# Kernel optimization log

Measured on AMD Instinct MI355X. Metric: run time of the kernel, lower is better.

The kernel has to match this reference:

```python
import jax, jax.numpy as jnp
import numpy as np

N = 50000        # nodes
E = 800000       # edges (avg degree 16)
H = 128          # hidden_nf
IN_NODE = 11     # in_node_nf
IN_EDGE = 4      # in_edge_nf
L = 4            # n_layers


def _lin_init(key, fan_in, fan_out, layers=None):
    shape = (fan_in, fan_out) if layers is None else (layers, fan_in, fan_out)
    return jax.random.normal(key, shape, dtype=jnp.float32) / np.sqrt(fan_in)


def setup_inputs() -> dict:
    key = jax.random.key(0)
    ks = jax.random.split(key, 16)
    edge_in = 2 * H + 1 + IN_EDGE   # [h_row, h_col, radial, edge_attr]
    node_in = H + H + IN_NODE       # [h, agg, h0]
    return {
        "h0": jax.random.normal(ks[0], (N, IN_NODE), dtype=jnp.float32),
        "x": jax.random.normal(ks[1], (N, 3), dtype=jnp.float32),
        "edge_index": jax.random.randint(ks[2], (2, E), 0, N),
        "edge_attr": jax.random.normal(ks[3], (E, IN_EDGE), dtype=jnp.float32),
        "node_mask": jnp.ones((N, 1), dtype=jnp.float32),
        "edge_mask": jnp.ones((E, 1), dtype=jnp.float32),
        "n_nodes": N,
        "emb_w": _lin_init(ks[4], IN_NODE, H),
        "emb_b": jnp.zeros((H,), dtype=jnp.float32),
        "ew1": _lin_init(ks[5], edge_in, H, L),
        "eb1": jnp.zeros((L, H), dtype=jnp.float32),
        "ew2": _lin_init(ks[6], H, H, L),
        "eb2": jnp.zeros((L, H), dtype=jnp.float32),
        "nw1": _lin_init(ks[7], node_in, H, L),
        "nb1": jnp.zeros((L, H), dtype=jnp.float32),
        "nw2": _lin_init(ks[8], H, H, L),
        "nb2": jnp.zeros((L, H), dtype=jnp.float32),
    }


def reference(h0, x, edge_index, edge_attr, node_mask, edge_mask, n_nodes,
              emb_w, emb_b, ew1, eb1, ew2, eb2, nw1, nb1, nw2, nb2):
    row, col = edge_index[0], edge_index[1]
    num_nodes = h0.shape[0]
    # coord2radial (coords never updated since coord_model is not called)
    coord_diff = x[row] - x[col]                               # [E, 3]
    radial = jnp.sum(coord_diff * coord_diff, axis=1, keepdims=True)  # [E, 1]

    h = h0 @ emb_w + emb_b                                     # embedding, [N, H]
    for i in range(L):
        # edge model
        edge_in = jnp.concatenate([h[row], h[col], radial, edge_attr], axis=1)
        m = jax.nn.silu(edge_in @ ew1[i] + eb1[i])
        m = jax.nn.silu(m @ ew2[i] + eb2[i])
        m = m * edge_mask                                      # [E, H]
        # node model: scatter-sum messages, concat with h and node_attr=h0
        agg = jax.ops.segment_sum(m, row, num_segments=num_nodes)  # [N, H]
        node_in = jnp.concatenate([h, agg, h0], axis=1)
        out = jax.nn.silu(node_in @ nw1[i] + nb1[i]) @ nw2[i] + nb2[i]
        h = h + out                                            # recurrent residual
    return h
```

## Files before the change

kernel.cpp:

```cpp
#include <hip/hip_runtime.h>

#define NN 50000
#define NE 800000
#define HD 128
#define INN 11
#define NL 4
#define NG16 3125
#define BTS 132
#define K1S 292
#define NB  196

typedef __attribute__((ext_vector_type(8))) short bf16x8;
typedef __attribute__((ext_vector_type(4))) float f32x4;
typedef __attribute__((ext_vector_type(2))) float f32x2;

__device__ __forceinline__ float silu_f(float x) {
    return x * __builtin_amdgcn_rcpf(1.0f + __expf(-x));
}

__device__ __forceinline__ short f2bf(float x) {
    unsigned u = __float_as_uint(x);
    return (short)((u + 0x7FFFu + ((u >> 16) & 1u)) >> 16);
}
__device__ __forceinline__ unsigned f2bf2u(float lo, float hi) {
    unsigned a = __float_as_uint(lo), b = __float_as_uint(hi);
    a = (a + 0x7FFFu + ((a >> 16) & 1u)) >> 16;
    b = (b + 0x7FFFu + ((b >> 16) & 1u)) & 0xFFFF0000u;
    return a | b;
}
__device__ __forceinline__ bf16x8 pack8(float4 a, float4 b) {
    bf16x8 r;
    r[0] = f2bf(a.x); r[1] = f2bf(a.y); r[2] = f2bf(a.z); r[3] = f2bf(a.w);
    r[4] = f2bf(b.x); r[5] = f2bf(b.y); r[6] = f2bf(b.z); r[7] = f2bf(b.w);
    return r;
}

__global__ __launch_bounds__(256) void embed_kernel(
    const float* __restrict__ h0, const float* __restrict__ w,
    const float* __restrict__ b, float* __restrict__ h)
{
    int idx = blockIdx.x * 256 + threadIdx.x;
    if (idx >= NN * HD) return;
    int n = idx >> 7, j = idx & 127;
    float acc = b[j];
    #pragma unroll
    for (int k = 0; k < INN; ++k)
        acc += h0[n * INN + k] * w[k * HD + j];
    h[idx] = acc;
}

__global__ __launch_bounds__(256) void csr_zero(int* __restrict__ cnt)
{
    int i = blockIdx.x * 256 + threadIdx.x;
    if (i < NN) cnt[i] = 0;
}

__global__ __launch_bounds__(256) void csr_hist(const int* __restrict__ ei, int* __restrict__ cnt)
{
    int e = blockIdx.x * 256 + threadIdx.x;
    atomicAdd(&cnt[ei[e]], 1);
}

__global__ __launch_bounds__(256) void csr_blocksum(
    const int* __restrict__ cnt, int* __restrict__ bsum)
{
    __shared__ int red[4];
    int j = blockIdx.x * 256 + threadIdx.x;
    int v = (j < NN) ? cnt[j] : 0;
    #pragma unroll
    for (int off = 1; off < 64; off <<= 1) v += __shfl_xor(v, off, 64);
    int lane = threadIdx.x & 63, wv = threadIdx.x >> 6;
    if (lane == 0) red[wv] = v;
    __syncthreads();
    if (threadIdx.x == 0)
        bsum[blockIdx.x] = red[0] + red[1] + red[2] + red[3];
}

__global__ __launch_bounds__(256) void csr_scanpart(
    const int* __restrict__ bsum, int* __restrict__ boff, int* __restrict__ rowptr)
{
    __shared__ int part[256];
    int t = threadIdx.x;
    int v = (t < NB) ? bsum[t] : 0;
    part[t] = v;
    __syncthreads();
    #pragma unroll
    for (int off = 1; off < 256; off <<= 1) {
        int tmp = (t >= off) ? part[t - off] : 0;
        __syncthreads();
        part[t] += tmp;
        __syncthreads();
    }
    if (t < NB) boff[t] = part[t] - v;
    if (t == NB - 1) rowptr[NN] = part[t];
}

__global__ __launch_bounds__(256) void csr_emit(
    const int* __restrict__ cnt, const int* __restrict__ boff,
    int* __restrict__ rowptr, int* __restrict__ cursor)
{
    __shared__ int part[256];
    int t = threadIdx.x;
    int j = blockIdx.x * 256 + t;
    int v = (j < NN) ? cnt[j] : 0;
    part[t] = v;
    __syncthreads();
    #pragma unroll
    for (int off = 1; off < 256; off <<= 1) {
        int tmp = (t >= off) ? part[t - off] : 0;
        __syncthreads();
        part[t] += tmp;
        __syncthreads();
    }
    if (j < NN) {
        int r = boff[blockIdx.x] + part[t] - v;
        rowptr[j] = r;
        cursor[j] = r;
    }
}

__global__ __launch_bounds__(256) void csr_fill(
    const int* __restrict__ ei, int* __restrict__ cursor, int* __restrict__ eidx)
{
    int e = blockIdx.x * 256 + threadIdx.x;
    int r = ei[e];
    int p = atomicAdd(&cursor[r], 1);
    eidx[p] = e;
}

__global__ __launch_bounds__(256) void edge_pre(
    const int* __restrict__ ei, const int* __restrict__ eidx,
    const float* __restrict__ x, const float* __restrict__ emask,
    int4* __restrict__ ed_p)
{
    int p = blockIdx.x * 256 + threadIdx.x;
    int e = eidx[p];
    int r = ei[e], c = ei[NE + e];
    float dx = x[3 * r]     - x[3 * c];
    float dy = x[3 * r + 1] - x[3 * c + 1];
    float dz = x[3 * r + 2] - x[3 * c + 2];
    float rad = dx * dx + dy * dy + dz * dz;
    ed_p[p] = make_int4(r * 64, c * 64, __float_as_int(rad), __float_as_int(emask[e]));
}

__global__ __launch_bounds__(1024) void vpad_zero(unsigned* __restrict__ vb32)
{
    vb32[(size_t)NE * 64 + threadIdx.x] = 0u;
}

__global__ __launch_bounds__(512) void tu_mfma(
    const float* __restrict__ h, const float* __restrict__ ew1_l,
    const float* __restrict__ eb1_l,
    short* __restrict__ tb, short* __restrict__ ub)
{
    __shared__ __align__(16) short BT[128 * BTS];
    const float* wsrc = ew1_l + (blockIdx.y ? 128 * HD : 0);
    short* outp = blockIdx.y ? ub : tb;
    for (int i = threadIdx.x; i < 128 * 128; i += 512) {
        int c = i >> 7, k = i & 127;
        BT[c * BTS + k] = f2bf(wsrc[k * HD + c]);
    }
    int wv = threadIdx.x >> 6, lane = threadIdx.x & 63;
    int ln15 = lane & 15, quad = lane >> 4;
    __syncthreads();

    for (int g = blockIdx.x * 8 + wv; g < NG16; g += gridDim.x * 8) {
        int row = g * 16 + ln15;
        const float* hrow = h + row * HD;
        bf16x8 afr[4];
        #pragma unroll
        for (int kt = 0; kt < 4; ++kt) {
            float4 x0 = *(const float4*)(hrow + kt * 32 + quad * 8);
            float4 x1 = *(const float4*)(hrow + kt * 32 + quad * 8 + 4);
            afr[kt] = pack8(x0, x1);
        }
        #pragma unroll
        for (int ct = 0; ct < 8; ++ct) {
            f32x4 acc = {0.f, 0.f, 0.f, 0.f};
            #pragma unroll
            for (int kt = 0; kt < 4; ++kt) {
                bf16x8 bfr = *(const bf16x8*)&BT[(ct * 16 + ln15) * BTS + kt * 32 + quad * 8];
                acc = __builtin_amdgcn_mfma_f32_16x16x32_bf16(afr[kt], bfr, acc, 0, 0, 0);
            }
            int col = ct * 16 + ln15;
            float bb = blockIdx.y ? 0.f : eb1_l[col];
            #pragma unroll
            for (int r4 = 0; r4 < 4; ++r4) {
                int orow = g * 16 + quad * 4 + r4;
                outp[orow * HD + col] = f2bf(acc[r4] + bb);
            }
        }
    }
}

__global__ __launch_bounds__(512) void edge_v_kernel(
    const short* __restrict__ tb, const short* __restrict__ ub,
    const int4* __restrict__ ed_p, const int* __restrict__ eidx,
    const float* __restrict__ eattr,
    const float* __restrict__ ew1_l,
    short* __restrict__ vbuf)
{
    int cp = threadIdx.x & 63;
    int c0 = cp * 2;
    f32x2 wr2  = *(const f32x2*)&ew1_l[256 * HD + c0];
    f32x2 wa02 = *(const f32x2*)&ew1_l[257 * HD + c0];
    f32x2 wa12 = *(const f32x2*)&ew1_l[258 * HD + c0];
    f32x2 wa22 = *(const f32x2*)&ew1_l[259 * HD + c0];
    f32x2 wa32 = *(const f32x2*)&ew1_l[260 * HD + c0];

    const unsigned* tb32 = (const unsigned*)tb;
    const unsigned* ub32 = (const unsigned*)ub;
    const float4*   ea4  = (const float4*)eattr;
    unsigned*       vb32 = (unsigned*)vbuf;

    int w  = (blockIdx.x * 512 + threadIdx.x) >> 6;
    int nw = gridDim.x * 8;

    for (int p0 = w * 4; p0 < NE; p0 += nw * 4) {
        int4 edv[4]; unsigned twv[4], uwv[4]; float4 eav[4];
        #pragma unroll
        for (int j = 0; j < 4; ++j) edv[j] = ed_p[p0 + j];
        #pragma unroll
        for (int j = 0; j < 4; ++j) {
            twv[j] = tb32[edv[j].x + cp];
            uwv[j] = ub32[edv[j].y + cp];
            eav[j] = ea4[eidx[p0 + j]];
        }
        #pragma unroll
        for (int j = 0; j < 4; ++j) {
            float rad = __int_as_float(edv[j].z);
            f32x2 s;
            s.x = __uint_as_float(twv[j] << 16)        + __uint_as_float(uwv[j] << 16);
            s.y = __uint_as_float(twv[j] & 0xFFFF0000u) + __uint_as_float(uwv[j] & 0xFFFF0000u);
            s += rad * wr2;
            s += eav[j].x * wa02;
            s += eav[j].y * wa12;
            s += eav[j].z * wa22;
            s += eav[j].w * wa32;
            vb32[(size_t)(p0 + j) * 64 + cp] = f2bf2u(silu_f(s.x), silu_f(s.y));
        }
    }
}

__global__ __launch_bounds__(512) void edge_agg_kernel(
    const short* __restrict__ vbuf, const int4* __restrict__ ed_p,
    const int* __restrict__ rowptr,
    const float* __restrict__ ew2_l, const float* __restrict__ eb2_l,
    short* __restrict__ aggb)
{
    __shared__ __align__(16) short BT[128 * BTS];
    __shared__ float s_b2[128];

    for (int i = threadIdx.x; i < 128 * 128; i += 512) {
        int k = i >> 7, n = i & 127;
        BT[n * BTS + k] = f2bf(ew2_l[i]);
    }
    if (threadIdx.x < 128) s_b2[threadIdx.x] = eb2_l[threadIdx.x];

    int lane = threadIdx.x & 63;
    int wv   = threadIdx.x >> 6;
    int ln15 = lane & 15;
    int quad = lane >> 4;
    __syncthreads();

    for (int n = blockIdx.x * 8 + wv; n < NN; n += gridDim.x * 8) {
        int s = rowptr[n], en = rowptr[n + 1];

        float sums[8];
        #pragma unroll
        for (int ct = 0; ct < 8; ++ct) sums[ct] = 0.f;

        for (int base = s; base < en; base += 16) {
            const short* vrow = vbuf + (size_t)(base + ln15) * HD + quad * 8;
            bf16x8 afr[4];
            #pragma unroll
            for (int kt = 0; kt < 4; ++kt)
                afr[kt] = *(const bf16x8*)(vrow + kt * 32);

            int pr = base + quad * 4;
            float mk0 = (pr + 0 < en) ? __int_as_float(ed_p[pr + 0].w) : 0.f;
            float mk1 = (pr + 1 < en) ? __int_as_float(ed_p[pr + 1].w) : 0.f;
            float mk2 = (pr + 2 < en) ? __int_as_float(ed_p[pr + 2].w) : 0.f;
            float mk3 = (pr + 3 < en) ? __int_as_float(ed_p[pr + 3].w) : 0.f;

            #pragma unroll
            for (int ct = 0; ct < 8; ++ct) {
                f32x4 acc = {0.f, 0.f, 0.f, 0.f};
                #pragma unroll
                for (int kt = 0; kt < 4; ++kt) {
                    bf16x8 bfr = *(const bf16x8*)&BT[(ct * 16 + ln15) * BTS + kt * 32 + quad * 8];
                    acc = __builtin_amdgcn_mfma_f32_16x16x32_bf16(afr[kt], bfr, acc, 0, 0, 0);
                }
                float b2c = s_b2[ct * 16 + ln15];
                sums[ct] += silu_f(acc[0] + b2c) * mk0 + silu_f(acc[1] + b2c) * mk1
                          + silu_f(acc[2] + b2c) * mk2 + silu_f(acc[3] + b2c) * mk3;
            }
        }

        #pragma unroll
        for (int ct = 0; ct < 8; ++ct) {
            float v = sums[ct];
            v += __shfl_xor(v, 16, 64);
            v += __shfl_xor(v, 32, 64);
            sums[ct] = v;
        }
        float vA = (quad & 2) ? ((quad & 1) ? sums[6] : sums[4])
                              : ((quad & 1) ? sums[2] : sums[0]);
        float vB = (quad & 2) ? ((quad & 1) ? sums[7] : sums[5])
                              : ((quad & 1) ? sums[3] : sums[1]);
        int colA = quad * 32 + ln15;
        aggb[(size_t)n * HD + colA]      = f2bf(vA);
        aggb[(size_t)n * HD + colA + 16] = f2bf(vB);
    }
}

__global__ __launch_bounds__(512) void nk1_mfma(
    const float* __restrict__ h, const short* __restrict__ aggb,
    const float* __restrict__ h0,
    const float* __restrict__ nw1_l, const float* __restrict__ nb1_l,
    short* __restrict__ qb)
{
    __shared__ __align__(16) short BT[64 * K1S];
    int c0 = blockIdx.y * 64;
    for (int i = threadIdx.x; i < 64 * 288; i += 512) {
        int c = i / 288, k = i - c * 288;
        BT[c * K1S + k] = (k < 267) ? f2bf(nw1_l[k * HD + c0 + c]) : (short)0;
    }
    int wv = threadIdx.x >> 6, lane = threadIdx.x & 63;
    int ln15 = lane & 15, quad = lane >> 4;
    __syncthreads();

    for (int g = blockIdx.x * 8 + wv; g < NG16; g += gridDim.x * 8) {
        int row = g * 16 + ln15;
        const float* hrow = h + row * HD;
        bf16x8 afr[9];
        #pragma unroll
        for (int kt = 0; kt < 4; ++kt) {
            float4 x0 = *(const float4*)(hrow + kt * 32 + quad * 8);
            float4 x1 = *(const float4*)(hrow + kt * 32 + quad * 8 + 4);
            afr[kt] = pack8(x0, x1);
        }
        #pragma unroll
        for (int kt = 0; kt < 4; ++kt)
            afr[4 + kt] = *(const bf16x8*)(aggb + (size_t)row * HD + kt * 32 + quad * 8);
        {
            bf16x8 a8 = {0, 0, 0, 0, 0, 0, 0, 0};
            if (quad == 0) {
                #pragma unroll
                for (int jj = 0; jj < 8; ++jj) a8[jj] = f2bf(h0[row * INN + jj]);
            } else if (quad == 1) {
                #pragma unroll
                for (int jj = 0; jj < 3; ++jj) a8[jj] = f2bf(h0[row * INN + 8 + jj]);
            }
            afr[8] = a8;
        }
        #pragma unroll
        for (int ct = 0; ct < 4; ++ct) {
            f32x4 acc = {0.f, 0.f, 0.f, 0.f};
            #pragma unroll
            for (int kt = 0; kt < 9; ++kt) {
                bf16x8 bfr = *(const bf16x8*)&BT[(ct * 16 + ln15) * K1S + kt * 32 + quad * 8];
                acc = __builtin_amdgcn_mfma_f32_16x16x32_bf16(afr[kt], bfr, acc, 0, 0, 0);
            }
            int col = c0 + ct * 16 + ln15;
            float b = nb1_l[col];
            #pragma unroll
            for (int r4 = 0; r4 < 4; ++r4) {
                int orow = g * 16 + quad * 4 + r4;
                qb[orow * HD + col] = f2bf(silu_f(acc[r4] + b));
            }
        }
    }
}

__global__ __launch_bounds__(512) void nk2_mfma(
    const short* __restrict__ qb, const float* __restrict__ nw2_l,
    const float* __restrict__ nb2_l, float* __restrict__ h)
{
    __shared__ __align__(16) short BT[128 * BTS];
    for (int i = threadIdx.x; i < 128 * 128; i += 512) {
        int c = i >> 7, k = i & 127;
        BT[c * BTS + k] = f2bf(nw2_l[k * HD + c]);
    }
    int wv = threadIdx.x >> 6, lane = threadIdx.x & 63;
    int ln15 = lane & 15, quad = lane >> 4;
    __syncthreads();

    for (int g = blockIdx.x * 8 + wv; g < NG16; g += gridDim.x * 8) {
        int row = g * 16 + ln15;
        bf16x8 afr[4];
        #pragma unroll
        for (int kt = 0; kt < 4; ++kt)
            afr[kt] = *(const bf16x8*)(qb + row * HD + kt * 32 + quad * 8);

        #pragma unroll
        for (int ct = 0; ct < 8; ++ct) {
            f32x4 acc = {0.f, 0.f, 0.f, 0.f};
            #pragma unroll
            for (int kt = 0; kt < 4; ++kt) {
                bf16x8 bfr = *(const bf16x8*)&BT[(ct * 16 + ln15) * BTS + kt * 32 + quad * 8];
                acc = __builtin_amdgcn_mfma_f32_16x16x32_bf16(afr[kt], bfr, acc, 0, 0, 0);
            }
            int col = ct * 16 + ln15;
            float b = nb2_l[col];
            #pragma unroll
            for (int r4 = 0; r4 < 4; ++r4) {
                int orow = g * 16 + quad * 4 + r4;
                h[orow * HD + col] += acc[r4] + b;
            }
        }
    }
}

extern "C" void kernel_launch(void* const* d_in, const int* in_sizes, int n_in,
                              void* d_out, int out_size, void* d_ws, size_t ws_size,
                              hipStream_t stream)
{
    const float* h0    = (const float*)d_in[0];
    const float* x     = (const float*)d_in[1];
    const int*   ei    = (const int*)d_in[2];
    const float* eattr = (const float*)d_in[3];
    const float* emask = (const float*)d_in[5];
    const float* emb_w = (const float*)d_in[7];
    const float* emb_b = (const float*)d_in[8];
    const float* ew1   = (const float*)d_in[9];
    const float* eb1   = (const float*)d_in[10];
    const float* ew2   = (const float*)d_in[11];
    const float* eb2   = (const float*)d_in[12];
    const float* nw1   = (const float*)d_in[13];
    const float* nb1   = (const float*)d_in[14];
    const float* nw2   = (const float*)d_in[15];
    const float* nb2   = (const float*)d_in[16];

    float* h = (float*)d_out;

    short*  tb     = (short*)d_ws;
    short*  ub     = tb + (size_t)NN * HD;
    short*  aggb   = ub + (size_t)NN * HD;
    short*  vbuf   = aggb + (size_t)NN * HD;
    int4*   ed_p   = (int4*)(vbuf + (size_t)(NE + 16) * HD);
    int*    rowptr = (int*)(ed_p + NE);
    int*    cnt    = rowptr + NN + 1;
    int*    cursor = cnt + NN;
    int*    eidx   = cursor + NN;
    int*    bsum   = eidx + NE;
    int*    boff   = bsum + NB;
    short*  qb     = tb;

    csr_zero<<<(NN + 255) / 256, 256, 0, stream>>>(cnt);
    csr_hist<<<NE / 256, 256, 0, stream>>>(ei, cnt);
    csr_blocksum<<<NB, 256, 0, stream>>>(cnt, bsum);
    csr_scanpart<<<1, 256, 0, stream>>>(bsum, boff, rowptr);
    csr_emit<<<NB, 256, 0, stream>>>(cnt, boff, rowptr, cursor);
    csr_fill<<<NE / 256, 256, 0, stream>>>(ei, cursor, eidx);
    edge_pre<<<NE / 256, 256, 0, stream>>>(ei, eidx, x, emask, ed_p);
    vpad_zero<<<1, 1024, 0, stream>>>((unsigned*)vbuf);

    embed_kernel<<<(NN * HD + 255) / 256, 256, 0, stream>>>(h0, emb_w, emb_b, h);

    dim3 gtu(128, 2);
    dim3 gn1(128, 2);
    for (int l = 0; l < NL; ++l) {
        tu_mfma<<<gtu, 512, 0, stream>>>(h, ew1 + l * 261 * HD, eb1 + l * HD, tb, ub);
        edge_v_kernel<<<1024, 512, 0, stream>>>(tb, ub, ed_p, eidx, eattr,
            ew1 + l * 261 * HD, vbuf);
        edge_agg_kernel<<<1024, 512, 0, stream>>>(vbuf, ed_p, rowptr,
            ew2 + l * HD * HD, eb2 + l * HD, aggb);
        nk1_mfma<<<gn1, 512, 0, stream>>>(h, aggb, h0,
            nw1 + l * 267 * HD, nb1 + l * HD, qb);
        nk2_mfma<<<128, 512, 0, stream>>>(qb, nw2 + l * HD * HD, nb2 + l * HD, h);
    }
}
```

Before: 1.451 ms.

## Keep bf16 shadow of h and prepacked h0, fuse tu halves into one pass

```diff
diff --git a/kernel.cpp b/kernel.cpp
--- a/kernel.cpp
+++ b/kernel.cpp
@@ -37,7 +37,7 @@
 
 __global__ __launch_bounds__(256) void embed_kernel(
     const float* __restrict__ h0, const float* __restrict__ w,
-    const float* __restrict__ b, float* __restrict__ h)
+    const float* __restrict__ b, float* __restrict__ h, short* __restrict__ hb)
 {
     int idx = blockIdx.x * 256 + threadIdx.x;
     if (idx >= NN * HD) return;
@@ -47,6 +47,16 @@
     for (int k = 0; k < INN; ++k)
         acc += h0[n * INN + k] * w[k * HD + j];
     h[idx] = acc;
+    hb[idx] = f2bf(acc);
+}
+
+__global__ __launch_bounds__(256) void h0_pack(
+    const float* __restrict__ h0, short* __restrict__ h0b)
+{
+    int idx = blockIdx.x * 256 + threadIdx.x;
+    if (idx >= NN * 32) return;
+    int n = idx >> 5, j = idx & 31;
+    h0b[idx] = (j < INN) ? f2bf(h0[n * INN + j]) : (short)0;
 }
 
 __global__ __launch_bounds__(256) void csr_zero(int* __restrict__ cnt)
@@ -149,16 +159,16 @@
 }
 
 __global__ __launch_bounds__(512) void tu_mfma(
-    const float* __restrict__ h, const float* __restrict__ ew1_l,
+    const short* __restrict__ hb, const float* __restrict__ ew1_l,
     const float* __restrict__ eb1_l,
     short* __restrict__ tb, short* __restrict__ ub)
 {
-    __shared__ __align__(16) short BT[128 * BTS];
-    const float* wsrc = ew1_l + (blockIdx.y ? 128 * HD : 0);
-    short* outp = blockIdx.y ? ub : tb;
+    __shared__ __align__(16) short BTt[128 * BTS];
+    __shared__ __align__(16) short BTu[128 * BTS];
     for (int i = threadIdx.x; i < 128 * 128; i += 512) {
         int c = i >> 7, k = i & 127;
-        BT[c * BTS + k] = f2bf(wsrc[k * HD + c]);
+        BTt[c * BTS + k] = f2bf(ew1_l[k * HD + c]);
+        BTu[c * BTS + k] = f2bf(ew1_l[(128 + k) * HD + c]);
     }
     int wv = threadIdx.x >> 6, lane = threadIdx.x & 63;
     int ln15 = lane & 15, quad = lane >> 4;
@@ -166,28 +176,41 @@
 
     for (int g = blockIdx.x * 8 + wv; g < NG16; g += gridDim.x * 8) {
         int row = g * 16 + ln15;
-        const float* hrow = h + row * HD;
+        const short* hrow = hb + (size_t)row * HD + quad * 8;
         bf16x8 afr[4];
         #pragma unroll
-        for (int kt = 0; kt < 4; ++kt) {
-            float4 x0 = *(const float4*)(hrow + kt * 32 + quad * 8);
-            float4 x1 = *(const float4*)(hrow + kt * 32 + quad * 8 + 4);
-            afr[kt] = pack8(x0, x1);
-        }
+        for (int kt = 0; kt < 4; ++kt)
+            afr[kt] = *(const bf16x8*)(hrow + kt * 32);
+
         #pragma unroll
         for (int ct = 0; ct < 8; ++ct) {
             f32x4 acc = {0.f, 0.f, 0.f, 0.f};
             #pragma unroll
             for (int kt = 0; kt < 4; ++kt) {
-                bf16x8 bfr = *(const bf16x8*)&BT[(ct * 16 + ln15) * BTS + kt * 32 + quad * 8];
+                bf16x8 bfr = *(const bf16x8*)&BTt[(ct * 16 + ln15) * BTS + kt * 32 + quad * 8];
                 acc = __builtin_amdgcn_mfma_f32_16x16x32_bf16(afr[kt], bfr, acc, 0, 0, 0);
             }
             int col = ct * 16 + ln15;
-            float bb = blockIdx.y ? 0.f : eb1_l[col];
+            float bb = eb1_l[col];
             #pragma unroll
             for (int r4 = 0; r4 < 4; ++r4) {
                 int orow = g * 16 + quad * 4 + r4;
-                outp[orow * HD + col] = f2bf(acc[r4] + bb);
+                tb[orow * HD + col] = f2bf(acc[r4] + bb);
+            }
+        }
+        #pragma unroll
+        for (int ct = 0; ct < 8; ++ct) {
+            f32x4 acc = {0.f, 0.f, 0.f, 0.f};
+            #pragma unroll
+            for (int kt = 0; kt < 4; ++kt) {
+                bf16x8 bfr = *(const bf16x8*)&BTu[(ct * 16 + ln15) * BTS + kt * 32 + quad * 8];
+                acc = __builtin_amdgcn_mfma_f32_16x16x32_bf16(afr[kt], bfr, acc, 0, 0, 0);
+            }
+            int col = ct * 16 + ln15;
+            #pragma unroll
+            for (int r4 = 0; r4 < 4; ++r4) {
+                int orow = g * 16 + quad * 4 + r4;
+                ub[orow * HD + col] = f2bf(acc[r4]);
             }
         }
     }
@@ -249,18 +272,20 @@
     short* __restrict__ aggb)
 {
     __shared__ __align__(16) short BT[128 * BTS];
-    __shared__ float s_b2[128];
 
     for (int i = threadIdx.x; i < 128 * 128; i += 512) {
         int k = i >> 7, n = i & 127;
         BT[n * BTS + k] = f2bf(ew2_l[i]);
     }
-    if (threadIdx.x < 128) s_b2[threadIdx.x] = eb2_l[threadIdx.x];
 
     int lane = threadIdx.x & 63;
     int wv   = threadIdx.x >> 6;
     int ln15 = lane & 15;
     int quad = lane >> 4;
+
+    float b2r[8];
+    #pragma unroll
+    for (int ct = 0; ct < 8; ++ct) b2r[ct] = eb2_l[ct * 16 + ln15];
     __syncthreads();
 
     for (int n = blockIdx.x * 8 + wv; n < NN; n += gridDim.x * 8) {
@@ -291,7 +316,7 @@
                     bf16x8 bfr = *(const bf16x8*)&BT[(ct * 16 + ln15) * BTS + kt * 32 + quad * 8];
                     acc = __builtin_amdgcn_mfma_f32_16x16x32_bf16(afr[kt], bfr, acc, 0, 0, 0);
                 }
-                float b2c = s_b2[ct * 16 + ln15];
+                float b2c = b2r[ct];
                 sums[ct] += silu_f(acc[0] + b2c) * mk0 + silu_f(acc[1] + b2c) * mk1
                           + silu_f(acc[2] + b2c) * mk2 + silu_f(acc[3] + b2c) * mk3;
             }
@@ -316,7 +341,7 @@
 
 __global__ __launch_bounds__(512) void nk1_mfma(
     const float* __restrict__ h, const short* __restrict__ aggb,
-    const float* __restrict__ h0,
+    const short* __restrict__ h0b,
     const float* __restrict__ nw1_l, const float* __restrict__ nb1_l,
     short* __restrict__ qb)
 {
@@ -333,6 +358,7 @@
     for (int g = blockIdx.x * 8 + wv; g < NG16; g += gridDim.x * 8) {
         int row = g * 16 + ln15;
         const float* hrow = h + row * HD;
+        const short* arow = aggb + (size_t)row * HD + quad * 8;
         bf16x8 afr[9];
         #pragma unroll
         for (int kt = 0; kt < 4; ++kt) {
@@ -342,18 +368,9 @@
         }
         #pragma unroll
         for (int kt = 0; kt < 4; ++kt)
-            afr[4 + kt] = *(const bf16x8*)(aggb + (size_t)row * HD + kt * 32 + quad * 8);
-        {
-            bf16x8 a8 = {0, 0, 0, 0, 0, 0, 0, 0};
-            if (quad == 0) {
-                #pragma unroll
-                for (int jj = 0; jj < 8; ++jj) a8[jj] = f2bf(h0[row * INN + jj]);
-            } else if (quad == 1) {
-                #pragma unroll
-                for (int jj = 0; jj < 3; ++jj) a8[jj] = f2bf(h0[row * INN + 8 + jj]);
-            }
-            afr[8] = a8;
-        }
+            afr[4 + kt] = *(const bf16x8*)(arow + kt * 32);
+        afr[8] = *(const bf16x8*)(h0b + (size_t)row * 32 + quad * 8);
+
         #pragma unroll
         for (int ct = 0; ct < 4; ++ct) {
             f32x4 acc = {0.f, 0.f, 0.f, 0.f};
@@ -375,7 +392,7 @@
 
 __global__ __launch_bounds__(512) void nk2_mfma(
     const short* __restrict__ qb, const float* __restrict__ nw2_l,
-    const float* __restrict__ nb2_l, float* __restrict__ h)
+    const float* __restrict__ nb2_l, float* __restrict__ h, short* __restrict__ hb)
 {
     __shared__ __align__(16) short BT[128 * BTS];
     for (int i = threadIdx.x; i < 128 * 128; i += 512) {
@@ -406,7 +423,9 @@
             #pragma unroll
             for (int r4 = 0; r4 < 4; ++r4) {
                 int orow = g * 16 + quad * 4 + r4;
-                h[orow * HD + col] += acc[r4] + b;
+                float hv = h[orow * HD + col] + acc[r4] + b;
+                h[orow * HD + col]  = hv;
+                hb[orow * HD + col] = f2bf(hv);
             }
         }
     }
@@ -445,7 +464,9 @@
     int*    eidx   = cursor + NN;
     int*    bsum   = eidx + NE;
     int*    boff   = bsum + NB;
+    short*  h0b    = (short*)(boff + NB);
     short*  qb     = tb;
+    short*  hb     = vbuf;
 
     csr_zero<<<(NN + 255) / 256, 256, 0, stream>>>(cnt);
     csr_hist<<<NE / 256, 256, 0, stream>>>(ei, cnt);
@@ -455,19 +476,19 @@
     csr_fill<<<NE / 256, 256, 0, stream>>>(ei, cursor, eidx);
     edge_pre<<<NE / 256, 256, 0, stream>>>(ei, eidx, x, emask, ed_p);
     vpad_zero<<<1, 1024, 0, stream>>>((unsigned*)vbuf);
-
-    embed_kernel<<<(NN * HD + 255) / 256, 256, 0, stream>>>(h0, emb_w, emb_b, h);
-
-    dim3 gtu(128, 2);
+    h0_pack<<<(NN * 32 + 255) / 256, 256, 0, stream>>>(h0, h0b);
+
+    embed_kernel<<<(NN * HD + 255) / 256, 256, 0, stream>>>(h0, emb_w, emb_b, h, hb);
+
     dim3 gn1(128, 2);
     for (int l = 0; l < NL; ++l) {
-        tu_mfma<<<gtu, 512, 0, stream>>>(h, ew1 + l * 261 * HD, eb1 + l * HD, tb, ub);
+        tu_mfma<<<256, 512, 0, stream>>>(hb, ew1 + l * 261 * HD, eb1 + l * HD, tb, ub);
         edge_v_kernel<<<1024, 512, 0, stream>>>(tb, ub, ed_p, eidx, eattr,
             ew1 + l * 261 * HD, vbuf);
         edge_agg_kernel<<<1024, 512, 0, stream>>>(vbuf, ed_p, rowptr,
             ew2 + l * HD * HD, eb2 + l * HD, aggb);
-        nk1_mfma<<<gn1, 512, 0, stream>>>(h, aggb, h0,
+        nk1_mfma<<<gn1, 512, 0, stream>>>(h, aggb, h0b,
             nw1 + l * 267 * HD, nb1 + l * HD, qb);
-        nk2_mfma<<<128, 512, 0, stream>>>(qb, nw2 + l * HD * HD, nb2 + l * HD, h);
-    }
-}
+        nk2_mfma<<<128, 512, 0, stream>>>(qb, nw2 + l * HD * HD, nb2 + l * HD, h, hb);
+    }
+}
```

Result: slower. 1.553 ms (+7.1%).

## Fuse CSR fill with edge preprocessing and pre-permute packed edge attributes

Applied to the files above, without the earlier changes.

```diff
diff --git a/kernel.cpp b/kernel.cpp
--- a/kernel.cpp
+++ b/kernel.cpp
@@ -49,6 +49,15 @@
     h[idx] = acc;
 }
 
+__global__ __launch_bounds__(256) void h0_pack(
+    const float* __restrict__ h0, short* __restrict__ h0b)
+{
+    int idx = blockIdx.x * 256 + threadIdx.x;
+    if (idx >= NN * 32) return;
+    int n = idx >> 5, j = idx & 31;
+    h0b[idx] = (j < INN) ? f2bf(h0[n * INN + j]) : (short)0;
+}
+
 __global__ __launch_bounds__(256) void csr_zero(int* __restrict__ cnt)
 {
     int i = blockIdx.x * 256 + threadIdx.x;
@@ -119,28 +128,27 @@
     }
 }
 
-__global__ __launch_bounds__(256) void csr_fill(
-    const int* __restrict__ ei, int* __restrict__ cursor, int* __restrict__ eidx)
+__global__ __launch_bounds__(256) void csr_fill_pre(
+    const int* __restrict__ ei, int* __restrict__ cursor,
+    const float* __restrict__ x, const float* __restrict__ emask,
+    const float* __restrict__ eattr,
+    int4* __restrict__ ed_p, ushort4* __restrict__ ea_p)
 {
     int e = blockIdx.x * 256 + threadIdx.x;
-    int r = ei[e];
+    int r = ei[e], c = ei[NE + e];
     int p = atomicAdd(&cursor[r], 1);
-    eidx[p] = e;
-}
-
-__global__ __launch_bounds__(256) void edge_pre(
-    const int* __restrict__ ei, const int* __restrict__ eidx,
-    const float* __restrict__ x, const float* __restrict__ emask,
-    int4* __restrict__ ed_p)
-{
-    int p = blockIdx.x * 256 + threadIdx.x;
-    int e = eidx[p];
-    int r = ei[e], c = ei[NE + e];
     float dx = x[3 * r]     - x[3 * c];
     float dy = x[3 * r + 1] - x[3 * c + 1];
     float dz = x[3 * r + 2] - x[3 * c + 2];
     float rad = dx * dx + dy * dy + dz * dz;
     ed_p[p] = make_int4(r * 64, c * 64, __float_as_int(rad), __float_as_int(emask[e]));
+    float4 ea = ((const float4*)eattr)[e];
+    ushort4 eb;
+    eb.x = (unsigned short)f2bf(ea.x);
+    eb.y = (unsigned short)f2bf(ea.y);
+    eb.z = (unsigned short)f2bf(ea.z);
+    eb.w = (unsigned short)f2bf(ea.w);
+    ea_p[p] = eb;
 }
 
 __global__ __launch_bounds__(1024) void vpad_zero(unsigned* __restrict__ vb32)
@@ -195,8 +203,7 @@
 
 __global__ __launch_bounds__(512) void edge_v_kernel(
     const short* __restrict__ tb, const short* __restrict__ ub,
-    const int4* __restrict__ ed_p, const int* __restrict__ eidx,
-    const float* __restrict__ eattr,
+    const int4* __restrict__ ed_p, const ushort4* __restrict__ ea_p,
     const float* __restrict__ ew1_l,
     short* __restrict__ vbuf)
 {
@@ -210,33 +217,36 @@
 
     const unsigned* tb32 = (const unsigned*)tb;
     const unsigned* ub32 = (const unsigned*)ub;
-    const float4*   ea4  = (const float4*)eattr;
     unsigned*       vb32 = (unsigned*)vbuf;
 
     int w  = (blockIdx.x * 512 + threadIdx.x) >> 6;
     int nw = gridDim.x * 8;
 
     for (int p0 = w * 4; p0 < NE; p0 += nw * 4) {
-        int4 edv[4]; unsigned twv[4], uwv[4]; float4 eav[4];
+        int4 edv[4]; unsigned twv[4], uwv[4]; ushort4 eav[4];
         #pragma unroll
         for (int j = 0; j < 4; ++j) edv[j] = ed_p[p0 + j];
         #pragma unroll
         for (int j = 0; j < 4; ++j) {
             twv[j] = tb32[edv[j].x + cp];
             uwv[j] = ub32[edv[j].y + cp];
-            eav[j] = ea4[eidx[p0 + j]];
+            eav[j] = ea_p[p0 + j];
         }
         #pragma unroll
         for (int j = 0; j < 4; ++j) {
             float rad = __int_as_float(edv[j].z);
+            float e0 = __uint_as_float((unsigned)eav[j].x << 16);
+            float e1 = __uint_as_float((unsigned)eav[j].y << 16);
+            float e2 = __uint_as_float((unsigned)eav[j].z << 16);
+            float e3 = __uint_as_float((unsigned)eav[j].w << 16);
             f32x2 s;
             s.x = __uint_as_float(twv[j] << 16)        + __uint_as_float(uwv[j] << 16);
             s.y = __uint_as_float(twv[j] & 0xFFFF0000u) + __uint_as_float(uwv[j] & 0xFFFF0000u);
             s += rad * wr2;
-            s += eav[j].x * wa02;
-            s += eav[j].y * wa12;
-            s += eav[j].z * wa22;
-            s += eav[j].w * wa32;
+            s += e0 * wa02;
+            s += e1 * wa12;
+            s += e2 * wa22;
+            s += e3 * wa32;
             vb32[(size_t)(p0 + j) * 64 + cp] = f2bf2u(silu_f(s.x), silu_f(s.y));
         }
     }
@@ -249,18 +259,20 @@
     short* __restrict__ aggb)
 {
     __shared__ __align__(16) short BT[128 * BTS];
-    __shared__ float s_b2[128];
 
     for (int i = threadIdx.x; i < 128 * 128; i += 512) {
         int k = i >> 7, n = i & 127;
         BT[n * BTS + k] = f2bf(ew2_l[i]);
     }
-    if (threadIdx.x < 128) s_b2[threadIdx.x] = eb2_l[threadIdx.x];
 
     int lane = threadIdx.x & 63;
     int wv   = threadIdx.x >> 6;
     int ln15 = lane & 15;
     int quad = lane >> 4;
+
+    float b2r[8];
+    #pragma unroll
+    for (int ct = 0; ct < 8; ++ct) b2r[ct] = eb2_l[ct * 16 + ln15];
     __syncthreads();
 
     for (int n = blockIdx.x * 8 + wv; n < NN; n += gridDim.x * 8) {
@@ -291,7 +303,7 @@
                     bf16x8 bfr = *(const bf16x8*)&BT[(ct * 16 + ln15) * BTS + kt * 32 + quad * 8];
                     acc = __builtin_amdgcn_mfma_f32_16x16x32_bf16(afr[kt], bfr, acc, 0, 0, 0);
                 }
-                float b2c = s_b2[ct * 16 + ln15];
+                float b2c = b2r[ct];
                 sums[ct] += silu_f(acc[0] + b2c) * mk0 + silu_f(acc[1] + b2c) * mk1
                           + silu_f(acc[2] + b2c) * mk2 + silu_f(acc[3] + b2c) * mk3;
             }
@@ -316,7 +328,7 @@
 
 __global__ __launch_bounds__(512) void nk1_mfma(
     const float* __restrict__ h, const short* __restrict__ aggb,
-    const float* __restrict__ h0,
+    const short* __restrict__ h0b,
     const float* __restrict__ nw1_l, const float* __restrict__ nb1_l,
     short* __restrict__ qb)
 {
@@ -333,6 +345,7 @@
     for (int g = blockIdx.x * 8 + wv; g < NG16; g += gridDim.x * 8) {
         int row = g * 16 + ln15;
         const float* hrow = h + row * HD;
+        const short* arow = aggb + (size_t)row * HD + quad * 8;
         bf16x8 afr[9];
         #pragma unroll
         for (int kt = 0; kt < 4; ++kt) {
@@ -342,18 +355,9 @@
         }
         #pragma unroll
         for (int kt = 0; kt < 4; ++kt)
-            afr[4 + kt] = *(const bf16x8*)(aggb + (size_t)row * HD + kt * 32 + quad * 8);
-        {
-            bf16x8 a8 = {0, 0, 0, 0, 0, 0, 0, 0};
-            if (quad == 0) {
-                #pragma unroll
-                for (int jj = 0; jj < 8; ++jj) a8[jj] = f2bf(h0[row * INN + jj]);
-            } else if (quad == 1) {
-                #pragma unroll
-                for (int jj = 0; jj < 3; ++jj) a8[jj] = f2bf(h0[row * INN + 8 + jj]);
-            }
-            afr[8] = a8;
-        }
+            afr[4 + kt] = *(const bf16x8*)(arow + kt * 32);
+        afr[8] = *(const bf16x8*)(h0b + (size_t)row * 32 + quad * 8);
+
         #pragma unroll
         for (int ct = 0; ct < 4; ++ct) {
             f32x4 acc = {0.f, 0.f, 0.f, 0.f};
@@ -434,27 +438,28 @@
 
     float* h = (float*)d_out;
 
-    short*  tb     = (short*)d_ws;
-    short*  ub     = tb + (size_t)NN * HD;
-    short*  aggb   = ub + (size_t)NN * HD;
-    short*  vbuf   = aggb + (size_t)NN * HD;
-    int4*   ed_p   = (int4*)(vbuf + (size_t)(NE + 16) * HD);
-    int*    rowptr = (int*)(ed_p + NE);
-    int*    cnt    = rowptr + NN + 1;
-    int*    cursor = cnt + NN;
-    int*    eidx   = cursor + NN;
-    int*    bsum   = eidx + NE;
-    int*    boff   = bsum + NB;
-    short*  qb     = tb;
+    short*   tb     = (short*)d_ws;
+    short*   ub     = tb + (size_t)NN * HD;
+    short*   aggb   = ub + (size_t)NN * HD;
+    short*   vbuf   = aggb + (size_t)NN * HD;
+    int4*    ed_p   = (int4*)(vbuf + (size_t)(NE + 16) * HD);
+    ushort4* ea_p   = (ushort4*)(ed_p + NE);
+    int*     rowptr = (int*)(ea_p + NE);
+    int*     cnt    = rowptr + NN + 1;
+    int*     cursor = cnt + NN;
+    int*     bsum   = cursor + NN;
+    int*     boff   = bsum + NB;
+    short*   h0b    = (short*)(boff + NB);
+    short*   qb     = tb;
 
     csr_zero<<<(NN + 255) / 256, 256, 0, stream>>>(cnt);
     csr_hist<<<NE / 256, 256, 0, stream>>>(ei, cnt);
     csr_blocksum<<<NB, 256, 0, stream>>>(cnt, bsum);
     csr_scanpart<<<1, 256, 0, stream>>>(bsum, boff, rowptr);
     csr_emit<<<NB, 256, 0, stream>>>(cnt, boff, rowptr, cursor);
-    csr_fill<<<NE / 256, 256, 0, stream>>>(ei, cursor, eidx);
-    edge_pre<<<NE / 256, 256, 0, stream>>>(ei, eidx, x, emask, ed_p);
+    csr_fill_pre<<<NE / 256, 256, 0, stream>>>(ei, cursor, x, emask, eattr, ed_p, ea_p);
     vpad_zero<<<1, 1024, 0, stream>>>((unsigned*)vbuf);
+    h0_pack<<<(NN * 32 + 255) / 256, 256, 0, stream>>>(h0, h0b);
 
     embed_kernel<<<(NN * HD + 255) / 256, 256, 0, stream>>>(h0, emb_w, emb_b, h);
 
@@ -462,11 +467,11 @@
     dim3 gn1(128, 2);
     for (int l = 0; l < NL; ++l) {
         tu_mfma<<<gtu, 512, 0, stream>>>(h, ew1 + l * 261 * HD, eb1 + l * HD, tb, ub);
-        edge_v_kernel<<<1024, 512, 0, stream>>>(tb, ub, ed_p, eidx, eattr,
+        edge_v_kernel<<<1024, 512, 0, stream>>>(tb, ub, ed_p, ea_p,
             ew1 + l * 261 * HD, vbuf);
         edge_agg_kernel<<<1024, 512, 0, stream>>>(vbuf, ed_p, rowptr,
             ew2 + l * HD * HD, eb2 + l * HD, aggb);
-        nk1_mfma<<<gn1, 512, 0, stream>>>(h, aggb, h0,
+        nk1_mfma<<<gn1, 512, 0, stream>>>(h, aggb, h0b,
             nw1 + l * 267 * HD, nb1 + l * HD, qb);
         nk2_mfma<<<128, 512, 0, stream>>>(qb, nw2 + l * HD * HD, nb2 + l * HD, h);
     }
```

New measurement: 1.395 ms (median of 2 runs). 3.9% less time.
